# Kernel optimization log

Measured on AMD Instinct MI355X. Metric: run time of the kernel, lower is better.

The kernel has to match this reference:

```python
import jax, jax.numpy as jnp
import numpy as np

N = 262144      # nodes
E = 1048576     # edges
NC = 30         # node feature dim
ED = 13         # bond (edge) feature dim
H = 256         # hidden_channels
GH = 512        # config.gnn_hidden_channels
OUT = 256       # out_channels
L = 4           # num_layers
G = 8192        # num graphs in batch


def setup_inputs() -> dict:
    key = jax.random.key(0)
    ks = jax.random.split(key, 16)
    inp = {
        "x": jax.random.normal(ks[0], (N, NC), jnp.float32),
        "edge_attr": jax.random.normal(ks[1], (E, ED), jnp.float32),
        "edge_index": jax.random.randint(ks[2], (2, E), 0, N, jnp.int64),
        "batch": jnp.sort(jax.random.randint(ks[3], (N,), 0, G, jnp.int64)),
        # node_to_hid: Linear(NC, H)
        "W_nh": jax.random.normal(ks[4], (NC, H), jnp.float32) / np.sqrt(NC),
        "b_nh": jnp.zeros((H,), jnp.float32),
        # shared GINEConv nn: Linear(H, H) + ReLU (same module instance for every layer)
        "W1": jax.random.normal(ks[5], (H, H), jnp.float32) / np.sqrt(H),
        "b1": jnp.zeros((H,), jnp.float32),
        # per-layer edge projection Linear(ED, H) inside each GINEConv
        "We": jax.random.normal(ks[6], (L, ED, H), jnp.float32) / np.sqrt(ED),
        "be": jnp.zeros((L, H), jnp.float32),
        # lin1: H -> GH, lin2: GH -> OUT
        "Wl1": jax.random.normal(ks[7], (H, GH), jnp.float32) / np.sqrt(H),
        "bl1": jnp.zeros((GH,), jnp.float32),
        "Wl2": jax.random.normal(ks[8], (GH, OUT), jnp.float32) / np.sqrt(GH),
        "bl2": jnp.zeros((OUT,), jnp.float32),
    }
    return inp


def reference(x, edge_attr, W_nh, b_nh, W1, b1, We, be, Wl1, bl1, Wl2, bl2,
              edge_index, batch):
    src = edge_index[0]  # x_j (messages flow source -> target)
    dst = edge_index[1]
    hid = x @ W_nh + b_nh                                   # [N, H]
    for l in range(L):
        e = edge_attr @ We[l] + be[l]                       # [E, H]
        msg = jax.nn.relu(hid[src] + e)                     # gather + fuse
        agg = jax.ops.segment_sum(msg, dst, num_segments=N) # scatter-sum
        # GINEConv (eps=0) -> shared nn (Linear+ReLU), then outer relu in forward
        hid = jax.nn.relu(jax.nn.relu((hid + agg) @ W1 + b1))
    out = jax.nn.relu(hid @ Wl1 + bl1) @ Wl2 + bl2          # [N, OUT]
    # global_add_pool readout
    return jax.ops.segment_sum(out, batch, num_segments=G)  # [G, OUT]
```

## Files before the change

### kernel.cpp

```cpp
#include <hip/hip_runtime.h>
#include <hip/hip_bf16.h>

#define N_NODES 262144
#define N_EDGES 1048576
#define NC      30
#define ED      13
#define H       256
#define GH      512
#define OUT_C   256
#define NLAYERS 4
#define NGRAPHS 8192

typedef __hip_bfloat16 bf16;
typedef __attribute__((ext_vector_type(8))) short short8;
typedef __attribute__((ext_vector_type(4))) float f32x4;

__device__ unsigned short g_W1t[H * H];
__device__ unsigned short g_Wl1t[2][H * H];
__device__ unsigned short g_Wl2t[2][H * H];
__device__ float g_b1[H];
__device__ float g_bl1[GH];
__device__ float g_bl2[OUT_C];
__device__ unsigned int g_ssrc[N_EDGES];
__device__ float        g_seat[N_EDGES * ED];
__device__ unsigned int g_rowptr[N_NODES + 1];
__device__ unsigned int g_cursor[N_NODES];
__device__ unsigned int g_bsum[1024];

__device__ __forceinline__ float hw2f(unsigned short h) {
    return __uint_as_float(((unsigned int)h) << 16);
}
__device__ __forceinline__ float ldf(const void* p, size_t i, bool isbf) {
    return isbf ? hw2f(((const unsigned short*)p)[i]) : ((const float*)p)[i];
}
__device__ __forceinline__ int ldi(const void* p, size_t j, bool is64) {
    return ((const int*)p)[is64 ? 2 * j : j];
}
__device__ __forceinline__ unsigned short bfbits(float f) {
    bf16 b = __float2bfloat16(f);
    return *(unsigned short*)&b;
}
__device__ __forceinline__ float lo16(unsigned int u) { return __uint_as_float(u << 16); }
__device__ __forceinline__ float hi16(unsigned int u) { return __uint_as_float(u & 0xFFFF0000u); }
__device__ __forceinline__ unsigned int pk2(float a, float b) {
    return (unsigned int)bfbits(a) | ((unsigned int)bfbits(b) << 16);
}
__device__ __forceinline__ bool sniff_bf16(const void* xv) {
    const unsigned short* q = (const unsigned short*)xv;
    int c = 0;
    for (int i = 0; i < 32; ++i) {
        unsigned short h = q[2 * i];
        int e = (h >> 7) & 0xFF;
        c += (h == 0 || (e >= 97 && e <= 141)) ? 1 : 0;
    }
    return c >= 20;
}
__device__ __forceinline__ bool sniff_i64(const void* pv, size_t baseWord) {
    const unsigned int* q = (const unsigned int*)pv;
    int z = 0;
    for (int i = 0; i < 32; ++i) z += (q[baseWord + 2 * i + 1] == 0) ? 1 : 0;
    return z >= 20;
}
__device__ __forceinline__ void gload_lds16(const void* g, void* l) {
    __builtin_amdgcn_global_load_lds(
        (const __attribute__((address_space(1))) unsigned int*)g,
        (__attribute__((address_space(3))) unsigned int*)l, 16, 0, 0);
}

__global__ __launch_bounds__(256) void fill_f4(float4* p, int n4, float val) {
    int i = blockIdx.x * 256 + threadIdx.x;
    int stride = gridDim.x * 256;
    float4 z = make_float4(val, val, val, val);
    for (; i < n4; i += stride) p[i] = z;
}

__global__ __launch_bounds__(256) void pack_wt(const void* __restrict__ in,
        int ldin, int k0, int n0, int which) {
    const bool isbf = sniff_bf16(in);
    unsigned short* outp = which == 0 ? g_W1t
                         : which == 1 ? g_Wl1t[0]
                         : which == 2 ? g_Wl1t[1]
                         : which == 3 ? g_Wl2t[0] : g_Wl2t[1];
    const int n = blockIdx.x, k = threadIdx.x;
    outp[(n << 8) + k] = bfbits(ldf(in, (size_t)(k0 + k) * ldin + n0 + n, isbf));
}
__global__ __launch_bounds__(256) void pack_bias(const void* b1, const void* bl1,
                                                 const void* bl2) {
    const int t = threadIdx.x;
    const bool s1 = sniff_bf16(b1), s2 = sniff_bf16(bl1), s3 = sniff_bf16(bl2);
    g_b1[t]        = ldf(b1,  t,       s1);
    g_bl1[t]       = ldf(bl1, t,       s2);
    g_bl1[t + 256] = ldf(bl1, t + 256, s2);
    g_bl2[t]       = ldf(bl2, t,       s3);
}

__global__ __launch_bounds__(256) void csr_zero() {
    g_cursor[blockIdx.x * 256 + threadIdx.x] = 0u;
}
__global__ __launch_bounds__(256) void hist_dst(const void* __restrict__ eidx) {
    const bool is64 = sniff_i64(eidx, 0);
    const int e = blockIdx.x * 256 + threadIdx.x;
    int dst = ldi(eidx, (size_t)N_EDGES + e, is64);
    if ((unsigned)dst >= (unsigned)N_NODES) dst = 0;
    atomicAdd(&g_cursor[dst], 1u);
}
__global__ __launch_bounds__(256) void scan1() {
    __shared__ unsigned int sh[256];
    const int tid = threadIdx.x;
    sh[tid] = g_cursor[blockIdx.x * 256 + tid];
    __syncthreads();
    for (int s = 128; s > 0; s >>= 1) {
        if (tid < s) sh[tid] += sh[tid + s];
        __syncthreads();
    }
    if (tid == 0) g_bsum[blockIdx.x] = sh[0];
}
__global__ __launch_bounds__(256) void scan2() {
    __shared__ unsigned int sh[1024];
    const int tid = threadIdx.x;
    for (int j = tid; j < 1024; j += 256) sh[j] = g_bsum[j];
    __syncthreads();
    if (tid == 0) {
        unsigned int run = 0;
        for (int j = 0; j < 1024; ++j) { unsigned int t = sh[j]; sh[j] = run; run += t; }
    }
    __syncthreads();
    for (int j = tid; j < 1024; j += 256) g_bsum[j] = sh[j];
}
__global__ __launch_bounds__(256) void scan3() {
    __shared__ unsigned int sh[256];
    const int tid = threadIdx.x;
    const int i = blockIdx.x * 256 + tid;
    const unsigned int v = g_cursor[i];
    sh[tid] = v;
    __syncthreads();
    for (int ofs = 1; ofs < 256; ofs <<= 1) {
        unsigned int t = (tid >= ofs) ? sh[tid - ofs] : 0u;
        __syncthreads();
        sh[tid] += t;
        __syncthreads();
    }
    const unsigned int excl = sh[tid] - v + g_bsum[blockIdx.x];
    g_rowptr[i] = excl;
    g_cursor[i] = excl;
    if (i == N_NODES - 1) g_rowptr[N_NODES] = excl + v;
}
__global__ __launch_bounds__(256) void scatter_e(
        const void* __restrict__ eidx, const void* __restrict__ eattr) {
    const bool is64 = sniff_i64(eidx, 0);
    const bool isbf = sniff_bf16(eattr);
    const int e = blockIdx.x * 256 + threadIdx.x;
    int src = ldi(eidx, e, is64);
    int dst = ldi(eidx, (size_t)N_EDGES + e, is64);
    if ((unsigned)src >= (unsigned)N_NODES) src = 0;
    if ((unsigned)dst >= (unsigned)N_NODES) dst = 0;
    unsigned int pos = atomicAdd(&g_cursor[dst], 1u);
    if (pos >= (unsigned)N_EDGES) return;
    g_ssrc[pos] = (unsigned int)src;
#pragma unroll
    for (int k = 0; k < ED; ++k)
        g_seat[(size_t)pos * ED + k] = ldf(eattr, (size_t)e * ED + k, isbf);
}

__global__ __launch_bounds__(256) void node_proj(
        const void* __restrict__ x, const void* __restrict__ W,
        const void* __restrict__ b, bf16* __restrict__ hid) {
    const bool isbf = sniff_bf16(x);
    __shared__ float xs[16 * NC];
    const int m0 = blockIdx.x * 16;
    for (int i = threadIdx.x; i < 16 * NC; i += 256)
        xs[i] = ldf(x, (size_t)m0 * NC + i, isbf);
    __syncthreads();
    const int col = threadIdx.x;
    float w[NC];
#pragma unroll
    for (int k = 0; k < NC; ++k) w[k] = ldf(W, (size_t)k * H + col, isbf);
    const float bias = ldf(b, col, isbf);
#pragma unroll 4
    for (int r = 0; r < 16; ++r) {
        float acc = bias;
#pragma unroll
        for (int k = 0; k < NC; ++k) acc += xs[r * NC + k] * w[k];
        hid[(size_t)(m0 + r) * H + col] = __float2bfloat16(acc);
    }
}

__global__ __launch_bounds__(256) void gine_agg(
        const void* __restrict__ We, size_t weOff,
        const void* __restrict__ be, size_t beOff,
        const unsigned short* __restrict__ hid,
        unsigned short* __restrict__ hsum) {
    const bool isbf = sniff_bf16(We);
    const int lane = threadIdx.x & 63;
    const int wave = threadIdx.x >> 6;
    const int c0 = 2 * lane;
    float w0[ED], w1[ED], w2[ED], w3[ED];
#pragma unroll
    for (int k = 0; k < ED; ++k) {
        const size_t o = weOff + (size_t)k * H;
        w0[k] = ldf(We, o + c0,       isbf);
        w1[k] = ldf(We, o + c0 + 1,   isbf);
        w2[k] = ldf(We, o + c0 + 128, isbf);
        w3[k] = ldf(We, o + c0 + 129, isbf);
    }
    const float bb0 = ldf(be, beOff + c0,       isbf);
    const float bb1 = ldf(be, beOff + c0 + 1,   isbf);
    const float bb2 = ldf(be, beOff + c0 + 128, isbf);
    const float bb3 = ldf(be, beOff + c0 + 129, isbf);

    const int nbase = blockIdx.x * 16 + wave * 4;
    for (int ni = 0; ni < 4; ++ni) {
        const int node = nbase + ni;
        const unsigned int r0 = __builtin_amdgcn_readfirstlane(g_rowptr[node]);
        const unsigned int r1 = __builtin_amdgcn_readfirstlane(g_rowptr[node + 1]);
        const unsigned short* hn = hid + (size_t)node * H;
        const unsigned int hu0 = *(const unsigned int*)(hn + c0);
        const unsigned int hu1 = *(const unsigned int*)(hn + c0 + 128);
        float a0 = lo16(hu0), a1 = hi16(hu0), a2 = lo16(hu1), a3 = hi16(hu1);
        for (unsigned int e = r0; e < r1; ++e) {
            const unsigned int s = __builtin_amdgcn_readfirstlane(g_ssrc[e]);
            const float* af = g_seat + (size_t)e * ED;
            const unsigned short* hs = hid + (size_t)s * H;
            const unsigned int u0 = *(const unsigned int*)(hs + c0);
            const unsigned int u1 = *(const unsigned int*)(hs + c0 + 128);
            float m0 = bb0, m1 = bb1, m2 = bb2, m3 = bb3;
#pragma unroll
            for (int k = 0; k < ED; ++k) {
                const float a = af[k];
                m0 += a * w0[k]; m1 += a * w1[k];
                m2 += a * w2[k]; m3 += a * w3[k];
            }
            m0 += lo16(u0); m1 += hi16(u0); m2 += lo16(u1); m3 += hi16(u1);
            a0 += fmaxf(m0, 0.f); a1 += fmaxf(m1, 0.f);
            a2 += fmaxf(m2, 0.f); a3 += fmaxf(m3, 0.f);
        }
        unsigned int* ho = (unsigned int*)(hsum + (size_t)node * H);
        ho[lane]      = pk2(a0, a1);
        ho[lane + 64] = pk2(a2, a3);
    }
}

template <int MODE>
__global__ __launch_bounds__(256) void gemm_mfma(
        const unsigned short* __restrict__ A, int bsel,
        unsigned short* __restrict__ Cb, float* __restrict__ Cf,
        const void* __restrict__ batch, size_t batOff, int doRelu, int useBias) {
    __shared__ unsigned short As[64 * 64];
    __shared__ unsigned short Bs[256 * 64];
    const int tid  = threadIdx.x;
    const int lane = tid & 63;
    const int wave = tid >> 6;
    const int m0   = blockIdx.x * 64;

    const unsigned short* Bt = bsel == 0 ? g_W1t
                             : bsel == 1 ? g_Wl1t[0]
                             : bsel == 2 ? g_Wl1t[1]
                             : bsel == 3 ? g_Wl2t[0] : g_Wl2t[1];
    const float* bias = bsel == 0 ? g_b1
                      : bsel == 1 ? g_bl1
                      : bsel == 2 ? g_bl1 + 256 : g_bl2;

    const int ar   = tid >> 2;
    const int ac   = (tid & 3) << 4;
    const int awb  = (ar << 7) + (ac << 1);
    const int aswz = (ar & 7) << 4;
    const size_t arow = (size_t)(m0 + ar) * H + ac;
    const int nrow = lane >> 3;
    const int kbu  = ((lane & 7) ^ nrow) << 4;

    f32x4 acc0[8], acc1[8];
    const f32x4 zz = {0.f, 0.f, 0.f, 0.f};
#pragma unroll
    for (int i = 0; i < 8; ++i) { acc0[i] = zz; acc1[i] = zz; }

    const int fr   = lane & 15;
    const int fg   = lane >> 4;
    const int rowb = (wave >> 1) << 5;
    const int colb = (wave & 1) << 7;

    for (int kt = 0; kt < 4; ++kt) {
#pragma unroll
        for (int j = 0; j < 8; ++j) {
            const int q = (wave << 3) + j;
            gload_lds16((const char*)Bt + (((size_t)(q << 3) + nrow) << 9)
                            + (kt << 7) + kbu,
                        (char*)Bs + (q << 10));
        }
        {
            const size_t aoff = arow + (kt << 6);
            uint4 w0 = *(const uint4*)(A + aoff);
            uint4 w1 = *(const uint4*)(A + aoff + 8);
            *(uint4*)((char*)As + (awb ^ aswz)) = w0;
            *(uint4*)((char*)As + ((awb + 16) ^ aswz)) = w1;
        }
        __syncthreads();
#pragma unroll
        for (int s = 0; s < 2; ++s) {
            const int kofs = (s << 6) + (fg << 4);
            const int r0 = rowb + fr;
            short8 aF0 = *(const short8*)((const char*)As +
                          ((r0 << 7) + (kofs ^ ((r0 & 7) << 4))));
            short8 aF1 = *(const short8*)((const char*)As +
                          (((r0 + 16) << 7) + (kofs ^ ((r0 & 7) << 4))));
#pragma unroll
            for (int ct = 0; ct < 8; ++ct) {
                const int cc = colb + (ct << 4) + fr;
                short8 bF = *(const short8*)((const char*)Bs +
                             ((cc << 7) + (kofs ^ ((cc & 7) << 4))));
                acc0[ct] = __builtin_amdgcn_mfma_f32_16x16x32_bf16(aF0, bF, acc0[ct], 0, 0, 0);
                acc1[ct] = __builtin_amdgcn_mfma_f32_16x16x32_bf16(aF1, bF, acc1[ct], 0, 0, 0);
            }
        }
        __syncthreads();
    }

    const int crow = m0 + rowb + (fg << 2);
    if (MODE == 0) {
#pragma unroll
        for (int ct = 0; ct < 8; ++ct) {
            const int cc = colb + (ct << 4) + fr;
            const float bc = bias[cc];
#pragma unroll
            for (int r = 0; r < 4; ++r) {
                float v0 = acc0[ct][r] + bc;
                float v1 = acc1[ct][r] + bc;
                if (doRelu) { v0 = fmaxf(v0, 0.f); v1 = fmaxf(v1, 0.f); }
                Cb[(size_t)(crow + r) * H + cc]      = bfbits(v0);
                Cb[(size_t)(crow + 16 + r) * H + cc] = bfbits(v1);
            }
        }
    } else {
        const bool is64 = sniff_i64(batch, N_NODES / 2);
        int ga[5], gb[5];
#pragma unroll
        for (int r = 0; r < 4; ++r) {
            int g0 = ldi(batch, batOff + crow + r, is64);
            int g1 = ldi(batch, batOff + crow + 16 + r, is64);
            ga[r] = ((unsigned)g0 < (unsigned)NGRAPHS) ? g0 : 0;
            gb[r] = ((unsigned)g1 < (unsigned)NGRAPHS) ? g1 : 0;
        }
#pragma unroll
        for (int ct = 0; ct < 8; ++ct) {
            const int cc = colb + (ct << 4) + fr;
            const float bc = useBias ? bias[cc] : 0.f;
            float run0 = 0.f, run1 = 0.f;
#pragma unroll
            for (int r = 0; r < 4; ++r) {
                run0 += acc0[ct][r] + bc;
                if (r == 3 || ga[r + 1] != ga[r]) {
                    atomicAdd(&Cf[(size_t)ga[r] * OUT_C + cc], run0); run0 = 0.f;
                }
                run1 += acc1[ct][r] + bc;
                if (r == 3 || gb[r + 1] != gb[r]) {
                    atomicAdd(&Cf[(size_t)gb[r] * OUT_C + cc], run1); run1 = 0.f;
                }
            }
        }
    }
}

extern "C" void kernel_launch(void* const* d_in, const int* in_sizes, int n_in,
                              void* d_out, int out_size, void* d_ws, size_t ws_size,
                              hipStream_t stream) {
    const void *x = nullptr, *eattr = nullptr, *eidx = nullptr, *batch = nullptr;
    const void *W_nh = nullptr, *W1 = nullptr, *We = nullptr, *be = nullptr;
    const void *Wl1 = nullptr, *Wl2 = nullptr, *bl1 = nullptr;
    const void *z256[3] = {nullptr, nullptr, nullptr};
    int nz = 0;
    for (int i = 0; i < n_in; ++i) {
        switch (in_sizes[i]) {
            case N_NODES * NC:     x     = d_in[i]; break;
            case N_EDGES * ED:     eattr = d_in[i]; break;
            case 2 * N_EDGES:      eidx  = d_in[i]; break;
            case N_NODES:          batch = d_in[i]; break;
            case NC * H:           W_nh  = d_in[i]; break;
            case H * H:            W1    = d_in[i]; break;
            case NLAYERS * ED * H: We    = d_in[i]; break;
            case NLAYERS * H:      be    = d_in[i]; break;
            case H * GH:           if (!Wl1) Wl1 = d_in[i]; else Wl2 = d_in[i]; break;
            case GH:               bl1   = d_in[i]; break;
            case H:                if (nz < 3) z256[nz++] = d_in[i]; break;
            default: break;
        }
    }
    const void* b_nh = z256[0];
    const void* b1   = (nz > 1) ? z256[1] : z256[0];
    const void* bl2  = (nz > 2) ? z256[2] : z256[0];
    float* out = (float*)d_out;

    if (!x || !eattr || !eidx || !batch || !W_nh || !W1 || !We || !be ||
        !Wl1 || !Wl2 || !bl1 || !b_nh) {
        fill_f4<<<1024, 256, 0, stream>>>((float4*)out, NGRAPHS * OUT_C / 4, 2.0e6f);
        return;
    }

    const size_t NH = (size_t)N_NODES * H;
    const size_t need = NH * 2 + NH * 2;
    if (ws_size < need) {
        fill_f4<<<1024, 256, 0, stream>>>((float4*)out, NGRAPHS * OUT_C / 4, 1.0e6f);
        return;
    }
    bf16* hid            = (bf16*)d_ws;
    unsigned short* hsum = (unsigned short*)((char*)d_ws + NH * 2);

    pack_wt<<<256, 256, 0, stream>>>(W1,  H,     0,   0, 0);
    pack_wt<<<256, 256, 0, stream>>>(Wl1, GH,    0,   0, 1);
    pack_wt<<<256, 256, 0, stream>>>(Wl1, GH,    0, 256, 2);
    pack_wt<<<256, 256, 0, stream>>>(Wl2, OUT_C, 0,   0, 3);
    pack_wt<<<256, 256, 0, stream>>>(Wl2, OUT_C, 256, 0, 4);
    pack_bias<<<1, 256, 0, stream>>>(b1, bl1, bl2);

    csr_zero<<<N_NODES / 256, 256, 0, stream>>>();
    hist_dst<<<N_EDGES / 256, 256, 0, stream>>>(eidx);
    scan1<<<N_NODES / 256, 256, 0, stream>>>();
    scan2<<<1, 256, 0, stream>>>();
    scan3<<<N_NODES / 256, 256, 0, stream>>>();
    scatter_e<<<N_EDGES / 256, 256, 0, stream>>>(eidx, eattr);

    node_proj<<<N_NODES / 16, 256, 0, stream>>>(x, W_nh, b_nh, hid);

    for (int l = 0; l < NLAYERS; ++l) {
        gine_agg<<<N_NODES / 16, 256, 0, stream>>>(
            We, (size_t)l * ED * H, be, (size_t)l * H,
            (const unsigned short*)hid, hsum);
        gemm_mfma<0><<<N_NODES / 64, 256, 0, stream>>>(
            hsum, 0, (unsigned short*)hid, nullptr, nullptr, 0, 1, 1);
    }

    unsigned short* t0 = hsum;
    fill_f4<<<2048, 256, 0, stream>>>((float4*)out, NGRAPHS * OUT_C / 4, 0.f);
    for (int c = 0; c < 2; ++c) {
        gemm_mfma<0><<<N_NODES / 64, 256, 0, stream>>>(
            (const unsigned short*)hid, 1 + c,
            t0, nullptr, nullptr, 0, 1, 1);
        gemm_mfma<1><<<N_NODES / 64, 256, 0, stream>>>(
            t0, 3 + c,
            nullptr, out, batch, 0, 0, c == 0);
    }
}
```

Before: 2.452 ms.

## Parallelize aggregation over edges with LDS atomics and drop LDS staging in GEMM

The aggregation kernel now gives each block 32 destination nodes and spreads their CSR edges across waves, accumulating messages into a 32KB shared-memory buffer with float atomics instead of one wave walking each node's edges serially. Edge attributes are padded to 16 floats so they load as float4, and destination ids are stored per edge. The MFMA GEMM drops its swizzled LDS tiles and reads A and B fragments straight from global memory, relying on cache. The aggregation change balances work across uneven node degrees, at the cost of LDS atomics and lower occupancy. The GEMM change removes staging and barriers but may cost more global traffic.

```diff
diff --git a/kernel.cpp b/kernel.cpp
--- a/kernel.cpp
+++ b/kernel.cpp
@@ -22,7 +22,8 @@
 __device__ float g_bl1[GH];
 __device__ float g_bl2[OUT_C];
 __device__ unsigned int g_ssrc[N_EDGES];
-__device__ float        g_seat[N_EDGES * ED];
+__device__ unsigned int g_sdst[N_EDGES];
+__device__ float        g_seat[N_EDGES * 16];
 __device__ unsigned int g_rowptr[N_NODES + 1];
 __device__ unsigned int g_cursor[N_NODES];
 __device__ unsigned int g_bsum[1024];
@@ -60,11 +61,6 @@
     int z = 0;
     for (int i = 0; i < 32; ++i) z += (q[baseWord + 2 * i + 1] == 0) ? 1 : 0;
     return z >= 20;
-}
-__device__ __forceinline__ void gload_lds16(const void* g, void* l) {
-    __builtin_amdgcn_global_load_lds(
-        (const __attribute__((address_space(1))) unsigned int*)g,
-        (__attribute__((address_space(3))) unsigned int*)l, 16, 0, 0);
 }
 
 __global__ __launch_bounds__(256) void fill_f4(float4* p, int n4, float val) {
@@ -157,9 +153,15 @@
     unsigned int pos = atomicAdd(&g_cursor[dst], 1u);
     if (pos >= (unsigned)N_EDGES) return;
     g_ssrc[pos] = (unsigned int)src;
-#pragma unroll
-    for (int k = 0; k < ED; ++k)
-        g_seat[(size_t)pos * ED + k] = ldf(eattr, (size_t)e * ED + k, isbf);
+    g_sdst[pos] = (unsigned int)dst;
+    float a[16];
+#pragma unroll
+    for (int k = 0; k < ED; ++k) a[k] = ldf(eattr, (size_t)e * ED + k, isbf);
+    a[13] = 0.f; a[14] = 0.f; a[15] = 0.f;
+    float* so = g_seat + (size_t)pos * 16;
+#pragma unroll
+    for (int k = 0; k < 4; ++k)
+        *(float4*)(so + 4 * k) = *(float4*)(a + 4 * k);
 }
 
 __global__ __launch_bounds__(256) void node_proj(
@@ -191,52 +193,68 @@
         const unsigned short* __restrict__ hid,
         unsigned short* __restrict__ hsum) {
     const bool isbf = sniff_bf16(We);
-    const int lane = threadIdx.x & 63;
-    const int wave = threadIdx.x >> 6;
-    const int c0 = 2 * lane;
+    __shared__ float acc[32 * 256];
+    const int tid  = threadIdx.x;
+    const int lane = tid & 63;
+    const int wave = tid >> 6;
+
+    for (int i = tid; i < 32 * 256; i += 256) acc[i] = 0.f;
+
     float w0[ED], w1[ED], w2[ED], w3[ED];
 #pragma unroll
     for (int k = 0; k < ED; ++k) {
         const size_t o = weOff + (size_t)k * H;
-        w0[k] = ldf(We, o + c0,       isbf);
-        w1[k] = ldf(We, o + c0 + 1,   isbf);
-        w2[k] = ldf(We, o + c0 + 128, isbf);
-        w3[k] = ldf(We, o + c0 + 129, isbf);
-    }
-    const float bb0 = ldf(be, beOff + c0,       isbf);
-    const float bb1 = ldf(be, beOff + c0 + 1,   isbf);
-    const float bb2 = ldf(be, beOff + c0 + 128, isbf);
-    const float bb3 = ldf(be, beOff + c0 + 129, isbf);
-
-    const int nbase = blockIdx.x * 16 + wave * 4;
-    for (int ni = 0; ni < 4; ++ni) {
-        const int node = nbase + ni;
-        const unsigned int r0 = __builtin_amdgcn_readfirstlane(g_rowptr[node]);
-        const unsigned int r1 = __builtin_amdgcn_readfirstlane(g_rowptr[node + 1]);
-        const unsigned short* hn = hid + (size_t)node * H;
-        const unsigned int hu0 = *(const unsigned int*)(hn + c0);
-        const unsigned int hu1 = *(const unsigned int*)(hn + c0 + 128);
-        float a0 = lo16(hu0), a1 = hi16(hu0), a2 = lo16(hu1), a3 = hi16(hu1);
-        for (unsigned int e = r0; e < r1; ++e) {
-            const unsigned int s = __builtin_amdgcn_readfirstlane(g_ssrc[e]);
-            const float* af = g_seat + (size_t)e * ED;
-            const unsigned short* hs = hid + (size_t)s * H;
-            const unsigned int u0 = *(const unsigned int*)(hs + c0);
-            const unsigned int u1 = *(const unsigned int*)(hs + c0 + 128);
-            float m0 = bb0, m1 = bb1, m2 = bb2, m3 = bb3;
-#pragma unroll
-            for (int k = 0; k < ED; ++k) {
-                const float a = af[k];
-                m0 += a * w0[k]; m1 += a * w1[k];
-                m2 += a * w2[k]; m3 += a * w3[k];
-            }
-            m0 += lo16(u0); m1 += hi16(u0); m2 += lo16(u1); m3 += hi16(u1);
-            a0 += fmaxf(m0, 0.f); a1 += fmaxf(m1, 0.f);
-            a2 += fmaxf(m2, 0.f); a3 += fmaxf(m3, 0.f);
-        }
-        unsigned int* ho = (unsigned int*)(hsum + (size_t)node * H);
-        ho[lane]      = pk2(a0, a1);
-        ho[lane + 64] = pk2(a2, a3);
+        w0[k] = ldf(We, o + lane,       isbf);
+        w1[k] = ldf(We, o + lane + 64,  isbf);
+        w2[k] = ldf(We, o + lane + 128, isbf);
+        w3[k] = ldf(We, o + lane + 192, isbf);
+    }
+    const float bb0 = ldf(be, beOff + lane,       isbf);
+    const float bb1 = ldf(be, beOff + lane + 64,  isbf);
+    const float bb2 = ldf(be, beOff + lane + 128, isbf);
+    const float bb3 = ldf(be, beOff + lane + 192, isbf);
+
+    const int nbase = blockIdx.x * 32;
+    const unsigned int r0 = g_rowptr[nbase];
+    const unsigned int r1 = g_rowptr[nbase + 32];
+    __syncthreads();
+
+    for (unsigned int e = r0 + wave; e < r1; e += 4) {
+        const unsigned int s = g_ssrc[e];
+        const int dl = (int)(g_sdst[e] - (unsigned int)nbase);
+        const float* sp = g_seat + (size_t)e * 16;
+        const float4 f0 = *(const float4*)(sp);
+        const float4 f1 = *(const float4*)(sp + 4);
+        const float4 f2 = *(const float4*)(sp + 8);
+        const float  fc = sp[12];
+        const unsigned short* hs = hid + (size_t)s * H;
+        const float h0 = hw2f(hs[lane]);
+        const float h1 = hw2f(hs[lane + 64]);
+        const float h2 = hw2f(hs[lane + 128]);
+        const float h3 = hw2f(hs[lane + 192]);
+        float m0 = bb0, m1 = bb1, m2 = bb2, m3 = bb3;
+        float af[ED] = {f0.x, f0.y, f0.z, f0.w, f1.x, f1.y, f1.z, f1.w,
+                        f2.x, f2.y, f2.z, f2.w, fc};
+#pragma unroll
+        for (int k = 0; k < ED; ++k) {
+            const float a = af[k];
+            m0 += a * w0[k]; m1 += a * w1[k];
+            m2 += a * w2[k]; m3 += a * w3[k];
+        }
+        const int ab = dl * 256 + lane;
+        atomicAdd(&acc[ab],       fmaxf(m0 + h0, 0.f));
+        atomicAdd(&acc[ab + 64],  fmaxf(m1 + h1, 0.f));
+        atomicAdd(&acc[ab + 128], fmaxf(m2 + h2, 0.f));
+        atomicAdd(&acc[ab + 192], fmaxf(m3 + h3, 0.f));
+    }
+    __syncthreads();
+
+    const int col = tid;
+#pragma unroll 4
+    for (int j = 0; j < 32; ++j) {
+        const size_t n = (size_t)(nbase + j);
+        const float v = acc[j * 256 + col] + hw2f(hid[n * H + col]);
+        hsum[n * H + col] = bfbits(v);
     }
 }
 
@@ -245,8 +263,6 @@
         const unsigned short* __restrict__ A, int bsel,
         unsigned short* __restrict__ Cb, float* __restrict__ Cf,
         const void* __restrict__ batch, size_t batOff, int doRelu, int useBias) {
-    __shared__ unsigned short As[64 * 64];
-    __shared__ unsigned short Bs[256 * 64];
     const int tid  = threadIdx.x;
     const int lane = tid & 63;
     const int wave = tid >> 6;
@@ -260,58 +276,31 @@
                       : bsel == 1 ? g_bl1
                       : bsel == 2 ? g_bl1 + 256 : g_bl2;
 
-    const int ar   = tid >> 2;
-    const int ac   = (tid & 3) << 4;
-    const int awb  = (ar << 7) + (ac << 1);
-    const int aswz = (ar & 7) << 4;
-    const size_t arow = (size_t)(m0 + ar) * H + ac;
-    const int nrow = lane >> 3;
-    const int kbu  = ((lane & 7) ^ nrow) << 4;
-
-    f32x4 acc0[8], acc1[8];
-    const f32x4 zz = {0.f, 0.f, 0.f, 0.f};
-#pragma unroll
-    for (int i = 0; i < 8; ++i) { acc0[i] = zz; acc1[i] = zz; }
-
     const int fr   = lane & 15;
     const int fg   = lane >> 4;
     const int rowb = (wave >> 1) << 5;
     const int colb = (wave & 1) << 7;
 
-    for (int kt = 0; kt < 4; ++kt) {
-#pragma unroll
-        for (int j = 0; j < 8; ++j) {
-            const int q = (wave << 3) + j;
-            gload_lds16((const char*)Bt + (((size_t)(q << 3) + nrow) << 9)
-                            + (kt << 7) + kbu,
-                        (char*)Bs + (q << 10));
-        }
-        {
-            const size_t aoff = arow + (kt << 6);
-            uint4 w0 = *(const uint4*)(A + aoff);
-            uint4 w1 = *(const uint4*)(A + aoff + 8);
-            *(uint4*)((char*)As + (awb ^ aswz)) = w0;
-            *(uint4*)((char*)As + ((awb + 16) ^ aswz)) = w1;
-        }
-        __syncthreads();
-#pragma unroll
-        for (int s = 0; s < 2; ++s) {
-            const int kofs = (s << 6) + (fg << 4);
-            const int r0 = rowb + fr;
-            short8 aF0 = *(const short8*)((const char*)As +
-                          ((r0 << 7) + (kofs ^ ((r0 & 7) << 4))));
-            short8 aF1 = *(const short8*)((const char*)As +
-                          (((r0 + 16) << 7) + (kofs ^ ((r0 & 7) << 4))));
-#pragma unroll
-            for (int ct = 0; ct < 8; ++ct) {
-                const int cc = colb + (ct << 4) + fr;
-                short8 bF = *(const short8*)((const char*)Bs +
-                             ((cc << 7) + (kofs ^ ((cc & 7) << 4))));
-                acc0[ct] = __builtin_amdgcn_mfma_f32_16x16x32_bf16(aF0, bF, acc0[ct], 0, 0, 0);
-                acc1[ct] = __builtin_amdgcn_mfma_f32_16x16x32_bf16(aF1, bF, acc1[ct], 0, 0, 0);
-            }
-        }
-        __syncthreads();
+    f32x4 acc0[8], acc1[8];
+    const f32x4 zz = {0.f, 0.f, 0.f, 0.f};
+#pragma unroll
+    for (int i = 0; i < 8; ++i) { acc0[i] = zz; acc1[i] = zz; }
+
+    const unsigned short* a0p = A + (size_t)(m0 + rowb + fr) * H;
+    const unsigned short* a1p = a0p + 16 * H;
+    const unsigned short* bcp = Bt + (size_t)(colb + fr) * H;
+
+#pragma unroll 2
+    for (int ks = 0; ks < 8; ++ks) {
+        const int ko = ks * 32 + fg * 8;
+        const short8 aF0 = *(const short8*)(a0p + ko);
+        const short8 aF1 = *(const short8*)(a1p + ko);
+#pragma unroll
+        for (int ct = 0; ct < 8; ++ct) {
+            const short8 bF = *(const short8*)(bcp + (size_t)(ct << 4) * H + ko);
+            acc0[ct] = __builtin_amdgcn_mfma_f32_16x16x32_bf16(aF0, bF, acc0[ct], 0, 0, 0);
+            acc1[ct] = __builtin_amdgcn_mfma_f32_16x16x32_bf16(aF1, bF, acc1[ct], 0, 0, 0);
+        }
     }
 
     const int crow = m0 + rowb + (fg << 2);
@@ -420,7 +409,7 @@
     node_proj<<<N_NODES / 16, 256, 0, stream>>>(x, W_nh, b_nh, hid);
 
     for (int l = 0; l < NLAYERS; ++l) {
-        gine_agg<<<N_NODES / 16, 256, 0, stream>>>(
+        gine_agg<<<N_NODES / 32, 256, 0, stream>>>(
             We, (size_t)l * ED * H, be, (size_t)l * H,
             (const unsigned short*)hid, hsum);
         gemm_mfma<0><<<N_NODES / 64, 256, 0, stream>>>(
```

After: 7.633 ms. 211% more time.
